# Performance work log

Hardware: AMD Instinct MI355X
Metric: run time of the kernel (lower is better)

The kernel has to match this reference:

```python
import jax, jax.numpy as jnp
import numpy as np

B, N, K, H, D = 2, 8192, 16, 4, 32
C_IN, C_OUT = 64, 128
HD = H * D


def setup_inputs() -> dict:
    key = jax.random.key(0)
    ks = jax.random.split(key, 16)
    s = 0.02
    return {
        "xyzs": jax.random.normal(ks[0], (B, N, 3), jnp.float32),
        "features": jax.random.normal(ks[1], (B, N, C_IN), jnp.float32),
        "k_graph": jax.random.randint(ks[2], (B, N, K), 0, N),
        # projections (stored as [in, out]; torch Linear applies x @ W.T)
        "Wk": jax.random.normal(ks[3], (C_IN, HD), jnp.float32) * s,
        "Wv": jax.random.normal(ks[4], (C_IN, HD), jnp.float32) * s,
        "Wq": jax.random.normal(ks[5], (C_IN, HD), jnp.float32) * s,
        # aggregate MLP: Linear(HD,HD) -> ReLU -> Linear(HD,H)
        "A1": jax.random.normal(ks[6], (HD, HD), jnp.float32) * s,
        "b1": jnp.zeros((HD,), jnp.float32),
        "A2": jax.random.normal(ks[7], (HD, H), jnp.float32) * s,
        "b2": jnp.zeros((H,), jnp.float32),
        # position MLP: Linear(3,3) -> ReLU -> Linear(3,HD)
        "P1": jax.random.normal(ks[8], (3, 3), jnp.float32) * s,
        "bp1": jnp.zeros((3,), jnp.float32),
        "P2": jax.random.normal(ks[9], (3, HD), jnp.float32) * s,
        "bp2": jnp.zeros((HD,), jnp.float32),
        # output projection Linear(HD, C_OUT)
        "Wout": jax.random.normal(ks[10], (HD, C_OUT), jnp.float32) * s,
        "bout": jnp.zeros((C_OUT,), jnp.float32),
    }


def reference(xyzs, features, k_graph, Wk, Wv, Wq, A1, b1, A2, b2,
              P1, bp1, P2, bp2, Wout, bout):
    # KNN gather (irregular access): [B,N,K,*]
    nbr_feat = jax.vmap(lambda f, g: f[g])(features, k_graph)   # [B,N,K,C_IN]
    nbr_xyz = jax.vmap(lambda x, g: x[g])(xyzs, k_graph)        # [B,N,K,3]

    rel_pos = xyzs[:, :, None, :] - nbr_xyz                      # [B,N,K,3]
    pe = jax.nn.relu(rel_pos @ P1 + bp1) @ P2 + bp2              # [B,N,K,HD]

    keys = nbr_feat @ Wk                                         # [B,N,K,HD]
    values = nbr_feat @ Wv                                       # [B,N,K,HD]
    queries = features @ Wq                                      # [B,N,HD]

    # subtraction attention + aggregate MLP -> per-head logits
    attn = queries[:, :, None, :] - keys + pe                    # [B,N,K,HD]
    attn = jax.nn.relu(attn @ A1 + b1) @ A2 + b2                 # [B,N,K,H]
    attn = jax.nn.softmax(attn, axis=-2)                         # softmax over K

    # weighted reduce over neighbors
    fv = (values + pe).reshape(B, N, K, H, D)
    fused = jnp.sum(attn[..., None] * fv, axis=2)                # [B,N,H,D]
    fused = fused.reshape(B, N, HD)
    return fused @ Wout + bout                                   # [B,N,C_OUT]
```

## Files before the change

### kernel.cpp

```cpp
#include <hip/hip_runtime.h>
#include <hip/hip_bf16.h>

#define BATCH 2
#define NPTS  8192
#define BN    (BATCH * NPTS)
#define KNN   16
#define HEADS 4
#define HD    128
#define CIN   64
#define COUT  128
#define WCOLS 384

using short8  = __attribute__((ext_vector_type(8))) short;
using float4v = __attribute__((ext_vector_type(4))) float;

static __device__ __forceinline__ unsigned short f2bf(float x) {
    unsigned u = __float_as_uint(x);
    u += 0x7fffu + ((u >> 16) & 1u);
    return (unsigned short)(u >> 16);
}
static __device__ __forceinline__ float bf_lo(unsigned u) { return __uint_as_float(u << 16); }
static __device__ __forceinline__ float bf_hi(unsigned u) { return __uint_as_float(u & 0xffff0000u); }
static __device__ __forceinline__ unsigned pack2(float a, float b) {
    return (unsigned)f2bf(a) | ((unsigned)f2bf(b) << 16);
}

template <int CTRL>
static __device__ __forceinline__ float dpp_mov(float x) {
    return __int_as_float(
        __builtin_amdgcn_update_dpp(0, __float_as_int(x), CTRL, 0xf, 0xf, false));
}
static __device__ __forceinline__ float ror_sum16(float x) {
    x += dpp_mov<0x128>(x);
    x += dpp_mov<0x124>(x);
    x += dpp_mov<0x122>(x);
    x += dpp_mov<0x121>(x);
    return x;
}
static __device__ __forceinline__ float ror_max16(float x) {
    x = fmaxf(x, dpp_mov<0x128>(x));
    x = fmaxf(x, dpp_mov<0x124>(x));
    x = fmaxf(x, dpp_mov<0x122>(x));
    x = fmaxf(x, dpp_mov<0x121>(x));
    return x;
}

__global__ __launch_bounds__(256) void prep_kernel(
        const float* __restrict__ Wk, const float* __restrict__ Wv,
        const float* __restrict__ Wq, const float* __restrict__ A1,
        const float* __restrict__ b1, const float* __restrict__ P2,
        const float* __restrict__ bp2, const float* __restrict__ Wout,
        unsigned short* __restrict__ WcatT, unsigned short* __restrict__ WoutT,
        float* __restrict__ P2A1, float* __restrict__ cvec) {
    int W = blockIdx.x * 4 + (threadIdx.x >> 6);
    int lane = threadIdx.x & 63;
    if (W < 384) {
        int kk = W / 6, nb = W % 6;
        int n = nb * 64 + lane;
        if (nb < 4) {
            const float* src = (nb < 2 ? Wq : Wk) + kk * HD;
            int jj = n & (HD - 1);
            float acc = 0.f;
            #pragma unroll 8
            for (int m = 0; m < HD; ++m)
                acc += src[m] * A1[m * HD + jj];
            WcatT[n * CIN + kk] = f2bf(acc);
        } else {
            WcatT[n * CIN + kk] = f2bf(Wv[kk * HD + (n - 2 * HD)]);
        }
    } else if (W < 384 + 256) {
        int u = (W - 384) * 64 + lane;
        int n = u >> 7, kk = u & 127;
        WoutT[u] = f2bf(Wout[kk * COUT + n]);
    } else if (W < 646) {
        int u = (W - 640) * 64 + lane;
        int r = u >> 7, j = u & 127;
        const float* src = P2 + r * HD;
        float acc = 0.f;
        #pragma unroll 8
        for (int m = 0; m < HD; ++m)
            acc += src[m] * A1[m * HD + j];
        P2A1[u] = acc;
    } else {
        int j = (W - 646) * 64 + lane;
        float acc = b1[j];
        #pragma unroll 8
        for (int m = 0; m < HD; ++m)
            acc += bp2[m] * A1[m * HD + j];
        cvec[j] = acc;
    }
}

#define AK 88
__global__ __launch_bounds__(256) void qkv_kernel(const float* __restrict__ F,
                                                  const unsigned short* __restrict__ WcatT,
                                                  const float* __restrict__ cvec,
                                                  unsigned short* __restrict__ QKVb) {
    __shared__ unsigned short Af[64 * AK];
    int p0 = blockIdx.x * 64;
    int t = threadIdx.x;

    #pragma unroll
    for (int i = 0; i < 4; ++i) {
        int v = t + i * 256;
        int row = v >> 4, c4 = (v & 15) * 4;
        float4 fa = *(const float4*)(F + (p0 + row) * CIN + c4);
        *(uint2*)(&Af[row * AK + c4]) = make_uint2(pack2(fa.x, fa.y), pack2(fa.z, fa.w));
    }
    __syncthreads();

    int w = t >> 6, l = t & 63;
    int ml = l & 15, quad = l >> 4;
    int n0 = w * 96;

    short8 b[6][2];
    #pragma unroll
    for (int j = 0; j < 6; ++j) {
        int n = n0 + j * 16 + ml;
        b[j][0] = *(const short8*)(WcatT + n * CIN + quad * 8);
        b[j][1] = *(const short8*)(WcatT + n * CIN + 32 + quad * 8);
    }
    short8 a[4][2];
    #pragma unroll
    for (int mt = 0; mt < 4; ++mt) {
        a[mt][0] = *(const short8*)(&Af[(mt * 16 + ml) * AK + quad * 8]);
        a[mt][1] = *(const short8*)(&Af[(mt * 16 + ml) * AK + 32 + quad * 8]);
    }

    #pragma unroll
    for (int j = 0; j < 6; ++j) {
        #pragma unroll
        for (int mt = 0; mt < 4; ++mt) {
            float4v acc = {0.f, 0.f, 0.f, 0.f};
            acc = __builtin_amdgcn_mfma_f32_16x16x32_bf16(b[j][0], a[mt][0], acc, 0, 0, 0);
            acc = __builtin_amdgcn_mfma_f32_16x16x32_bf16(b[j][1], a[mt][1], acc, 0, 0, 0);
            int nc = n0 + j * 16 + quad * 4;
            float c0 = 0.f, c1 = 0.f, c2 = 0.f, c3 = 0.f;
            if (nc < HD) {
                float4 cv = *(const float4*)(cvec + nc);
                c0 = cv.x; c1 = cv.y; c2 = cv.z; c3 = cv.w;
            }
            int row = p0 + mt * 16 + ml;
            *(uint2*)(QKVb + row * WCOLS + nc) =
                make_uint2(pack2(acc[0] + c0, acc[1] + c1),
                           pack2(acc[2] + c2, acc[3] + c3));
        }
    }
}

__global__ __launch_bounds__(256) void attn_kernel(
        const float* __restrict__ xyzs, const int* __restrict__ kg,
        const unsigned short* __restrict__ QKVb,
        const float* __restrict__ P1, const float* __restrict__ bp1,
        const float* __restrict__ P2, const float* __restrict__ bp2,
        const float* __restrict__ P2A1,
        const float* __restrict__ A2, const float* __restrict__ b2,
        unsigned short* __restrict__ FUSEDb) {
    int p = blockIdx.x;
    int b = p >> 13;
    int t = threadIdx.x;
    int g = t >> 4, k = t & 15, c0 = g * 8;
    int w = t >> 6;
    int lane = t & 63;

    __shared__ float4 A2s[HD];
    __shared__ float4 lgp[4][16];
    __shared__ float4 hs16[16];
    __shared__ float  ats[64];
    __shared__ float4 hbf[4];

    if (t < HD) A2s[t] = *(const float4*)(A2 + t * 4);

    int idx = kg[p * KNN + k];
    int q = b * NPTS + idx;

    float r0 = xyzs[p*3+0] - xyzs[q*3+0];
    float r1 = xyzs[p*3+1] - xyzs[q*3+1];
    float r2 = xyzs[p*3+2] - xyzs[q*3+2];
    float h0 = fmaxf(r0*P1[0] + r1*P1[3] + r2*P1[6] + bp1[0], 0.f);
    float h1 = fmaxf(r0*P1[1] + r1*P1[4] + r2*P1[7] + bp1[1], 0.f);
    float h2 = fmaxf(r0*P1[2] + r1*P1[5] + r2*P1[8] + bp1[2], 0.f);
    if (g == 0) hs16[k] = make_float4(h0, h1, h2, 0.f);

    uint4 qu = *(const uint4*)(QKVb + p * WCOLS + c0);
    uint4 ku = *(const uint4*)(QKVb + q * WCOLS + HD + c0);
    uint4 vu = *(const uint4*)(QKVb + q * WCOLS + 2 * HD + c0);

    float qz[8] = { bf_lo(qu.x), bf_hi(qu.x), bf_lo(qu.y), bf_hi(qu.y),
                    bf_lo(qu.z), bf_hi(qu.z), bf_lo(qu.w), bf_hi(qu.w) };
    float kr[8] = { bf_lo(ku.x), bf_hi(ku.x), bf_lo(ku.y), bf_hi(ku.y),
                    bf_lo(ku.z), bf_hi(ku.z), bf_lo(ku.w), bf_hi(ku.w) };

    float wa0[8], wa1[8], wa2[8];
    *(float4*)(wa0)     = *(const float4*)(P2A1 + 0*HD + c0);
    *(float4*)(wa0 + 4) = *(const float4*)(P2A1 + 0*HD + c0 + 4);
    *(float4*)(wa1)     = *(const float4*)(P2A1 + 1*HD + c0);
    *(float4*)(wa1 + 4) = *(const float4*)(P2A1 + 1*HD + c0 + 4);
    *(float4*)(wa2)     = *(const float4*)(P2A1 + 2*HD + c0);
    *(float4*)(wa2 + 4) = *(const float4*)(P2A1 + 2*HD + c0 + 4);

    __syncthreads();

    float pl0 = 0.f, pl1 = 0.f, pl2 = 0.f, pl3 = 0.f;
    #pragma unroll
    for (int j = 0; j < 8; ++j) {
        float z = fmaxf(qz[j] - kr[j] + h0*wa0[j] + h1*wa1[j] + h2*wa2[j], 0.f);
        float4 ar = A2s[c0 + j];
        pl0 += z * ar.x; pl1 += z * ar.y; pl2 += z * ar.z; pl3 += z * ar.w;
    }
    pl0 += __shfl_xor(pl0, 16, 64); pl0 += __shfl_xor(pl0, 32, 64);
    pl1 += __shfl_xor(pl1, 16, 64); pl1 += __shfl_xor(pl1, 32, 64);
    pl2 += __shfl_xor(pl2, 16, 64); pl2 += __shfl_xor(pl2, 32, 64);
    pl3 += __shfl_xor(pl3, 16, 64); pl3 += __shfl_xor(pl3, 32, 64);
    if (lane < 16) lgp[w][lane] = make_float4(pl0, pl1, pl2, pl3);
    __syncthreads();

    if (t < 64) {
        int hh = t >> 4, kk = t & 15;
        const float* lp = (const float*)lgp;
        float lgt = b2[hh] + lp[0*64 + kk*4 + hh] + lp[1*64 + kk*4 + hh]
                           + lp[2*64 + kk*4 + hh] + lp[3*64 + kk*4 + hh];
        float m = ror_max16(lgt);
        float e = __expf(lgt - m);
        float s = ror_sum16(e);
        float a = e / s;
        ats[t] = a;
        float4 hv = hs16[kk];
        float hb0 = ror_sum16(a * hv.x);
        float hb1 = ror_sum16(a * hv.y);
        float hb2 = ror_sum16(a * hv.z);
        if (kk == 0) hbf[hh] = make_float4(hb0, hb1, hb2, 0.f);
    }
    __syncthreads();

    float a = ats[w * 16 + k];
    float vr[8] = { bf_lo(vu.x), bf_hi(vu.x), bf_lo(vu.y), bf_hi(vu.y),
                    bf_lo(vu.z), bf_hi(vu.z), bf_lo(vu.w), bf_hi(vu.w) };
    float wv[8];
    #pragma unroll
    for (int j = 0; j < 8; ++j) wv[j] = ror_sum16(a * vr[j]);

    if (k == 0) {
        float4 hb = hbf[w];
        float q0[8], q1[8], q2[8], bpv[8];
        *(float4*)(q0)     = *(const float4*)(P2 + 0*HD + c0);
        *(float4*)(q0 + 4) = *(const float4*)(P2 + 0*HD + c0 + 4);
        *(float4*)(q1)     = *(const float4*)(P2 + 1*HD + c0);
        *(float4*)(q1 + 4) = *(const float4*)(P2 + 1*HD + c0 + 4);
        *(float4*)(q2)     = *(const float4*)(P2 + 2*HD + c0);
        *(float4*)(q2 + 4) = *(const float4*)(P2 + 2*HD + c0 + 4);
        *(float4*)(bpv)     = *(const float4*)(bp2 + c0);
        *(float4*)(bpv + 4) = *(const float4*)(bp2 + c0 + 4);
        float f[8];
        #pragma unroll
        for (int j = 0; j < 8; ++j)
            f[j] = wv[j] + hb.x*q0[j] + hb.y*q1[j] + hb.z*q2[j] + bpv[j];
        uint4 fu;
        fu.x = pack2(f[0], f[1]); fu.y = pack2(f[2], f[3]);
        fu.z = pack2(f[4], f[5]); fu.w = pack2(f[6], f[7]);
        *(uint4*)(FUSEDb + p * HD + c0) = fu;
    }
}

#define OK2 144
__global__ __launch_bounds__(256) void out_kernel(const unsigned short* __restrict__ FUSEDb,
                                                  const unsigned short* __restrict__ WoutT,
                                                  const float* __restrict__ bout,
                                                  float* __restrict__ out) {
    __shared__ unsigned short Af[64 * OK2];
    int p0 = blockIdx.x * 64;
    int t = threadIdx.x;

    #pragma unroll
    for (int i = 0; i < 4; ++i) {
        int v = t + i * 256;
        int row = v >> 4, c8 = (v & 15) * 8;
        *(uint4*)(&Af[row * OK2 + c8]) = *(const uint4*)(FUSEDb + (p0 + row) * HD + c8);
    }
    __syncthreads();

    int w = t >> 6, l = t & 63;
    int ml = l & 15, quad = l >> 4;
    int n0 = w * 32;

    short8 b[2][4];
    #pragma unroll
    for (int j = 0; j < 2; ++j) {
        int n = n0 + j * 16 + ml;
        #pragma unroll
        for (int ks = 0; ks < 4; ++ks)
            b[j][ks] = *(const short8*)(WoutT + n * HD + ks * 32 + quad * 8);
    }
    short8 a[4][4];
    #pragma unroll
    for (int mt = 0; mt < 4; ++mt)
        #pragma unroll
        for (int ks = 0; ks < 4; ++ks)
            a[mt][ks] = *(const short8*)(&Af[(mt * 16 + ml) * OK2 + ks * 32 + quad * 8]);

    #pragma unroll
    for (int j = 0; j < 2; ++j) {
        int nc = n0 + j * 16 + quad * 4;
        float4 bo = *(const float4*)(bout + nc);
        #pragma unroll
        for (int mt = 0; mt < 4; ++mt) {
            float4v acc = {0.f, 0.f, 0.f, 0.f};
            #pragma unroll
            for (int ks = 0; ks < 4; ++ks)
                acc = __builtin_amdgcn_mfma_f32_16x16x32_bf16(b[j][ks], a[mt][ks], acc, 0, 0, 0);
            int row = p0 + mt * 16 + ml;
            *(float4*)(out + row * COUT + nc) =
                make_float4(acc[0] + bo.x, acc[1] + bo.y, acc[2] + bo.z, acc[3] + bo.w);
        }
    }
}

extern "C" void kernel_launch(void* const* d_in, const int* in_sizes, int n_in,
                              void* d_out, int out_size, void* d_ws, size_t ws_size,
                              hipStream_t stream) {
    const float* xyzs = (const float*)d_in[0];
    const float* feat = (const float*)d_in[1];
    const int*   kg   = (const int*)  d_in[2];
    const float* Wk   = (const float*)d_in[3];
    const float* Wv   = (const float*)d_in[4];
    const float* Wq   = (const float*)d_in[5];
    const float* A1   = (const float*)d_in[6];
    const float* b1   = (const float*)d_in[7];
    const float* A2   = (const float*)d_in[8];
    const float* b2   = (const float*)d_in[9];
    const float* P1   = (const float*)d_in[10];
    const float* bp1  = (const float*)d_in[11];
    const float* P2   = (const float*)d_in[12];
    const float* bp2  = (const float*)d_in[13];
    const float* Wout = (const float*)d_in[14];
    const float* bout = (const float*)d_in[15];
    float* out = (float*)d_out;

    float* ws = (float*)d_ws;
    float* cvec = ws;
    float* P2A1 = ws + 128;
    unsigned short* QKVb  = (unsigned short*)(ws + 512);
    unsigned short* FUSEDb = QKVb + (size_t)BN * WCOLS;
    unsigned short* WcatT = FUSEDb + (size_t)BN * HD;
    unsigned short* WoutT = WcatT + WCOLS * CIN;

    prep_kernel<<<162, 256, 0, stream>>>(
        Wk, Wv, Wq, A1, b1, P2, bp2, Wout, WcatT, WoutT, P2A1, cvec);

    qkv_kernel<<<BN / 64, 256, 0, stream>>>(feat, WcatT, cvec, QKVb);

    attn_kernel<<<BN, 256, 0, stream>>>(
        xyzs, kg, QKVb, P1, bp1, P2, bp2, P2A1, A2, b2, FUSEDb);

    out_kernel<<<BN / 64, 256, 0, stream>>>(FUSEDb, WoutT, bout, out);
}
```

Baseline: 161.8 us.

## Fuse all four stages into one cooperative persistent kernel with grid syncs

Adds a cooperative mega-kernel of 1024 blocks that runs weight prep, QKV projection, attention and the output projection in sequence, with grid.sync between phases. Each block owns 16 points, prefetches the next point's neighbour data in software, and keeps fused results in LDS for an in-block MFMA output projection. This removes the launch gaps and the FUSED round-trip through global memory. In exchange it processes points serially per block with two block barriers per point, uses fewer blocks than the old one-block-per-point attention grid, and only runs if the occupancy check passes; otherwise it falls back to the four-kernel path.

```diff
diff --git a/kernel.cpp b/kernel.cpp
--- a/kernel.cpp
+++ b/kernel.cpp
@@ -1,5 +1,8 @@
 #include <hip/hip_runtime.h>
 #include <hip/hip_bf16.h>
+#include <hip/hip_cooperative_groups.h>
+
+namespace cg = cooperative_groups;
 
 #define BATCH 2
 #define NPTS  8192
@@ -43,6 +46,246 @@
     x = fmaxf(x, dpp_mov<0x122>(x));
     x = fmaxf(x, dpp_mov<0x121>(x));
     return x;
+}
+
+__global__ __launch_bounds__(256, 4) void mega_kernel(
+        const float* __restrict__ xyzs, const float* __restrict__ feat,
+        const int* __restrict__ kg,
+        const float* __restrict__ Wk, const float* __restrict__ Wv,
+        const float* __restrict__ Wq, const float* __restrict__ A1,
+        const float* __restrict__ b1, const float* __restrict__ A2,
+        const float* __restrict__ b2, const float* __restrict__ P1,
+        const float* __restrict__ bp1, const float* __restrict__ P2,
+        const float* __restrict__ bp2, const float* __restrict__ Wout,
+        const float* __restrict__ bout,
+        unsigned short* __restrict__ WcatT, unsigned short* __restrict__ WoutT,
+        float* __restrict__ P2A1, float* __restrict__ cvec,
+        unsigned short* __restrict__ QKVb, float* __restrict__ out) {
+    cg::grid_group grid = cg::this_grid();
+    int t = threadIdx.x;
+    int bid = blockIdx.x;
+    int w = t >> 6, lane = t & 63;
+
+    __shared__ unsigned short Af[16 * 88];
+    __shared__ float4 A2s[HD];
+    __shared__ float4 lgp[2][4][16];
+    __shared__ float4 hs16[2][16];
+    __shared__ float  ats[2][64];
+    __shared__ float4 hbf[2][4];
+    __shared__ unsigned short fusedLDS[16 * 136];
+
+    {
+        int W = bid * 4 + w;
+        if (W < 384) {
+            int kk = W / 6, nb = W % 6;
+            int n = nb * 64 + lane;
+            if (nb < 4) {
+                const float* src = (nb < 2 ? Wq : Wk) + kk * HD;
+                int jj = n & (HD - 1);
+                float acc = 0.f;
+                #pragma unroll 8
+                for (int m = 0; m < HD; ++m) acc += src[m] * A1[m * HD + jj];
+                WcatT[n * CIN + kk] = f2bf(acc);
+            } else {
+                WcatT[n * CIN + kk] = f2bf(Wv[kk * HD + (n - 2 * HD)]);
+            }
+        } else if (W < 640) {
+            int u = (W - 384) * 64 + lane;
+            int n = u >> 7, kk = u & 127;
+            WoutT[u] = f2bf(Wout[kk * COUT + n]);
+        } else if (W < 646) {
+            int u = (W - 640) * 64 + lane;
+            int r = u >> 7, jj = u & 127;
+            const float* src = P2 + r * HD;
+            float acc = 0.f;
+            #pragma unroll 8
+            for (int m = 0; m < HD; ++m) acc += src[m] * A1[m * HD + jj];
+            P2A1[u] = acc;
+        } else if (W < 648) {
+            int jj = (W - 646) * 64 + lane;
+            float acc = b1[jj];
+            #pragma unroll 8
+            for (int m = 0; m < HD; ++m) acc += bp2[m] * A1[m * HD + jj];
+            cvec[jj] = acc;
+        }
+    }
+    grid.sync();
+
+    int p0 = bid * 16;
+    {
+        {
+            int row = t >> 4, c4 = (t & 15) * 4;
+            float4 fa = *(const float4*)(feat + (p0 + row) * CIN + c4);
+            *(uint2*)(&Af[row * 88 + c4]) =
+                make_uint2(pack2(fa.x, fa.y), pack2(fa.z, fa.w));
+        }
+        __syncthreads();
+        int ml = lane & 15, quad = lane >> 4;
+        int n0 = w * 96;
+        short8 a0 = *(const short8*)(&Af[ml * 88 + quad * 8]);
+        short8 a1 = *(const short8*)(&Af[ml * 88 + 32 + quad * 8]);
+        #pragma unroll
+        for (int j = 0; j < 6; ++j) {
+            int n = n0 + j * 16 + ml;
+            short8 bf0 = *(const short8*)(WcatT + n * CIN + quad * 8);
+            short8 bf1 = *(const short8*)(WcatT + n * CIN + 32 + quad * 8);
+            float4v acc = {0.f, 0.f, 0.f, 0.f};
+            acc = __builtin_amdgcn_mfma_f32_16x16x32_bf16(bf0, a0, acc, 0, 0, 0);
+            acc = __builtin_amdgcn_mfma_f32_16x16x32_bf16(bf1, a1, acc, 0, 0, 0);
+            int nc = n0 + j * 16 + quad * 4;
+            float c0 = 0.f, c1 = 0.f, c2 = 0.f, c3 = 0.f;
+            if (nc < HD) {
+                float4 cv = *(const float4*)(cvec + nc);
+                c0 = cv.x; c1 = cv.y; c2 = cv.z; c3 = cv.w;
+            }
+            *(uint2*)(QKVb + (p0 + ml) * WCOLS + nc) =
+                make_uint2(pack2(acc[0] + c0, acc[1] + c1),
+                           pack2(acc[2] + c2, acc[3] + c3));
+        }
+    }
+    grid.sync();
+
+    {
+        int b = p0 >> 13;
+        int g = t >> 4, k = t & 15, c0g = g * 8;
+
+        if (t < HD) A2s[t] = *(const float4*)(A2 + t * 4);
+
+        float wa0[8], wa1[8], wa2[8];
+        *(float4*)(wa0)     = *(const float4*)(P2A1 + 0*HD + c0g);
+        *(float4*)(wa0 + 4) = *(const float4*)(P2A1 + 0*HD + c0g + 4);
+        *(float4*)(wa1)     = *(const float4*)(P2A1 + 1*HD + c0g);
+        *(float4*)(wa1 + 4) = *(const float4*)(P2A1 + 1*HD + c0g + 4);
+        *(float4*)(wa2)     = *(const float4*)(P2A1 + 2*HD + c0g);
+        *(float4*)(wa2 + 4) = *(const float4*)(P2A1 + 2*HD + c0g + 4);
+        __syncthreads();
+
+        int p = p0;
+        int idx = kg[p * KNN + k];
+        int q = b * NPTS + idx;
+        float xp0 = xyzs[p*3+0], xp1 = xyzs[p*3+1], xp2 = xyzs[p*3+2];
+        float xn0 = xyzs[q*3+0], xn1 = xyzs[q*3+1], xn2 = xyzs[q*3+2];
+        uint4 qu = *(const uint4*)(QKVb + p * WCOLS + c0g);
+        uint4 ku = *(const uint4*)(QKVb + q * WCOLS + HD + c0g);
+        uint4 vu = *(const uint4*)(QKVb + q * WCOLS + 2 * HD + c0g);
+
+        for (int j = 0; j < 16; ++j) {
+            int pr = j & 1;
+            float r0 = xp0 - xn0, r1 = xp1 - xn1, r2 = xp2 - xn2;
+            float h0 = fmaxf(r0*P1[0] + r1*P1[3] + r2*P1[6] + bp1[0], 0.f);
+            float h1 = fmaxf(r0*P1[1] + r1*P1[4] + r2*P1[7] + bp1[1], 0.f);
+            float h2 = fmaxf(r0*P1[2] + r1*P1[5] + r2*P1[8] + bp1[2], 0.f);
+            if (g == 0) hs16[pr][k] = make_float4(h0, h1, h2, 0.f);
+
+            int idxN = 0;
+            if (j < 15) idxN = kg[(p + 1) * KNN + k];
+
+            float qz[8] = { bf_lo(qu.x), bf_hi(qu.x), bf_lo(qu.y), bf_hi(qu.y),
+                            bf_lo(qu.z), bf_hi(qu.z), bf_lo(qu.w), bf_hi(qu.w) };
+            float kr[8] = { bf_lo(ku.x), bf_hi(ku.x), bf_lo(ku.y), bf_hi(ku.y),
+                            bf_lo(ku.z), bf_hi(ku.z), bf_lo(ku.w), bf_hi(ku.w) };
+            float pl0 = 0.f, pl1 = 0.f, pl2 = 0.f, pl3 = 0.f;
+            #pragma unroll
+            for (int jj = 0; jj < 8; ++jj) {
+                float z = fmaxf(qz[jj] - kr[jj] + h0*wa0[jj] + h1*wa1[jj] + h2*wa2[jj], 0.f);
+                float4 ar = A2s[c0g + jj];
+                pl0 += z * ar.x; pl1 += z * ar.y; pl2 += z * ar.z; pl3 += z * ar.w;
+            }
+            pl0 += __shfl_xor(pl0, 16, 64); pl0 += __shfl_xor(pl0, 32, 64);
+            pl1 += __shfl_xor(pl1, 16, 64); pl1 += __shfl_xor(pl1, 32, 64);
+            pl2 += __shfl_xor(pl2, 16, 64); pl2 += __shfl_xor(pl2, 32, 64);
+            pl3 += __shfl_xor(pl3, 16, 64); pl3 += __shfl_xor(pl3, 32, 64);
+            if (lane < 16) lgp[pr][w][lane] = make_float4(pl0, pl1, pl2, pl3);
+            __syncthreads();
+
+            if (t < 64) {
+                int hh = t >> 4, kk = t & 15;
+                const float* lp = (const float*)&lgp[pr][0][0];
+                float lgt = b2[hh] + lp[0*64 + kk*4 + hh] + lp[1*64 + kk*4 + hh]
+                                   + lp[2*64 + kk*4 + hh] + lp[3*64 + kk*4 + hh];
+                float m = ror_max16(lgt);
+                float e = __expf(lgt - m);
+                float s = ror_sum16(e);
+                float a = e / s;
+                ats[pr][t] = a;
+                float4 hv = hs16[pr][kk];
+                float hb0 = ror_sum16(a * hv.x);
+                float hb1 = ror_sum16(a * hv.y);
+                float hb2 = ror_sum16(a * hv.z);
+                if (kk == 0) hbf[pr][hh] = make_float4(hb0, hb1, hb2, 0.f);
+            }
+
+            uint4 quN, kuN, vuN;
+            float xp0N = 0.f, xp1N = 0.f, xp2N = 0.f;
+            float xn0N = 0.f, xn1N = 0.f, xn2N = 0.f;
+            int qN = b * NPTS + idxN;
+            if (j < 15) {
+                int pn = p + 1;
+                xp0N = xyzs[pn*3+0]; xp1N = xyzs[pn*3+1]; xp2N = xyzs[pn*3+2];
+                xn0N = xyzs[qN*3+0]; xn1N = xyzs[qN*3+1]; xn2N = xyzs[qN*3+2];
+                quN = *(const uint4*)(QKVb + pn * WCOLS + c0g);
+                kuN = *(const uint4*)(QKVb + qN * WCOLS + HD + c0g);
+                vuN = *(const uint4*)(QKVb + qN * WCOLS + 2 * HD + c0g);
+            }
+            __syncthreads();
+
+            float a = ats[pr][w * 16 + k];
+            float vr[8] = { bf_lo(vu.x), bf_hi(vu.x), bf_lo(vu.y), bf_hi(vu.y),
+                            bf_lo(vu.z), bf_hi(vu.z), bf_lo(vu.w), bf_hi(vu.w) };
+            float wv[8];
+            #pragma unroll
+            for (int jj = 0; jj < 8; ++jj) wv[jj] = ror_sum16(a * vr[jj]);
+
+            if (k == 0) {
+                float4 hb = hbf[pr][w];
+                float q0[8], q1[8], q2[8], bpv[8];
+                *(float4*)(q0)     = *(const float4*)(P2 + 0*HD + c0g);
+                *(float4*)(q0 + 4) = *(const float4*)(P2 + 0*HD + c0g + 4);
+                *(float4*)(q1)     = *(const float4*)(P2 + 1*HD + c0g);
+                *(float4*)(q1 + 4) = *(const float4*)(P2 + 1*HD + c0g + 4);
+                *(float4*)(q2)     = *(const float4*)(P2 + 2*HD + c0g);
+                *(float4*)(q2 + 4) = *(const float4*)(P2 + 2*HD + c0g + 4);
+                *(float4*)(bpv)     = *(const float4*)(bp2 + c0g);
+                *(float4*)(bpv + 4) = *(const float4*)(bp2 + c0g + 4);
+                float f[8];
+                #pragma unroll
+                for (int jj = 0; jj < 8; ++jj)
+                    f[jj] = wv[jj] + hb.x*q0[jj] + hb.y*q1[jj] + hb.z*q2[jj] + bpv[jj];
+                uint4 fu;
+                fu.x = pack2(f[0], f[1]); fu.y = pack2(f[2], f[3]);
+                fu.z = pack2(f[4], f[5]); fu.w = pack2(f[6], f[7]);
+                *(uint4*)(&fusedLDS[j * 136 + c0g]) = fu;
+            }
+
+            p += 1; q = qN;
+            qu = quN; ku = kuN; vu = vuN;
+            xp0 = xp0N; xp1 = xp1N; xp2 = xp2N;
+            xn0 = xn0N; xn1 = xn1N; xn2 = xn2N;
+        }
+        __syncthreads();
+
+        int ml = lane & 15, quad = lane >> 4;
+        short8 afr[4];
+        #pragma unroll
+        for (int ks = 0; ks < 4; ++ks)
+            afr[ks] = *(const short8*)(&fusedLDS[ml * 136 + ks * 32 + quad * 8]);
+        int n0 = w * 32;
+        #pragma unroll
+        for (int jn = 0; jn < 2; ++jn) {
+            int n = n0 + jn * 16 + ml;
+            float4v acc = {0.f, 0.f, 0.f, 0.f};
+            #pragma unroll
+            for (int ks = 0; ks < 4; ++ks) {
+                short8 bfr = *(const short8*)(WoutT + n * HD + ks * 32 + quad * 8);
+                acc = __builtin_amdgcn_mfma_f32_16x16x32_bf16(bfr, afr[ks], acc, 0, 0, 0);
+            }
+            int nc = n0 + jn * 16 + quad * 4;
+            float4 bo = *(const float4*)(bout + nc);
+            *(float4*)(out + (p0 + ml) * COUT + nc) =
+                make_float4(acc[0] + bo.x, acc[1] + bo.y,
+                            acc[2] + bo.z, acc[3] + bo.w);
+        }
+    }
 }
 
 __global__ __launch_bounds__(256) void prep_kernel(
@@ -62,13 +305,12 @@
             int jj = n & (HD - 1);
             float acc = 0.f;
             #pragma unroll 8
-            for (int m = 0; m < HD; ++m)
-                acc += src[m] * A1[m * HD + jj];
+            for (int m = 0; m < HD; ++m) acc += src[m] * A1[m * HD + jj];
             WcatT[n * CIN + kk] = f2bf(acc);
         } else {
             WcatT[n * CIN + kk] = f2bf(Wv[kk * HD + (n - 2 * HD)]);
         }
-    } else if (W < 384 + 256) {
+    } else if (W < 640) {
         int u = (W - 384) * 64 + lane;
         int n = u >> 7, kk = u & 127;
         WoutT[u] = f2bf(Wout[kk * COUT + n]);
@@ -78,15 +320,13 @@
         const float* src = P2 + r * HD;
         float acc = 0.f;
         #pragma unroll 8
-        for (int m = 0; m < HD; ++m)
-            acc += src[m] * A1[m * HD + j];
+        for (int m = 0; m < HD; ++m) acc += src[m] * A1[m * HD + j];
         P2A1[u] = acc;
-    } else {
+    } else if (W < 648) {
         int j = (W - 646) * 64 + lane;
         float acc = b1[j];
         #pragma unroll 8
-        for (int m = 0; m < HD; ++m)
-            acc += bp2[m] * A1[m * HD + j];
+        for (int m = 0; m < HD; ++m) acc += bp2[m] * A1[m * HD + j];
         cvec[j] = acc;
     }
 }
@@ -99,7 +339,6 @@
     __shared__ unsigned short Af[64 * AK];
     int p0 = blockIdx.x * 64;
     int t = threadIdx.x;
-
     #pragma unroll
     for (int i = 0; i < 4; ++i) {
         int v = t + i * 256;
@@ -108,11 +347,9 @@
         *(uint2*)(&Af[row * AK + c4]) = make_uint2(pack2(fa.x, fa.y), pack2(fa.z, fa.w));
     }
     __syncthreads();
-
     int w = t >> 6, l = t & 63;
     int ml = l & 15, quad = l >> 4;
     int n0 = w * 96;
-
     short8 b[6][2];
     #pragma unroll
     for (int j = 0; j < 6; ++j) {
@@ -126,7 +363,6 @@
         a[mt][0] = *(const short8*)(&Af[(mt * 16 + ml) * AK + quad * 8]);
         a[mt][1] = *(const short8*)(&Af[(mt * 16 + ml) * AK + 32 + quad * 8]);
     }
-
     #pragma unroll
     for (int j = 0; j < 6; ++j) {
         #pragma unroll
@@ -270,7 +506,6 @@
     __shared__ unsigned short Af[64 * OK2];
     int p0 = blockIdx.x * 64;
     int t = threadIdx.x;
-
     #pragma unroll
     for (int i = 0; i < 4; ++i) {
         int v = t + i * 256;
@@ -278,11 +513,9 @@
         *(uint4*)(&Af[row * OK2 + c8]) = *(const uint4*)(FUSEDb + (p0 + row) * HD + c8);
     }
     __syncthreads();
-
     int w = t >> 6, l = t & 63;
     int ml = l & 15, quad = l >> 4;
     int n0 = w * 32;
-
     short8 b[2][4];
     #pragma unroll
     for (int j = 0; j < 2; ++j) {
@@ -297,7 +530,6 @@
         #pragma unroll
         for (int ks = 0; ks < 4; ++ks)
             a[mt][ks] = *(const short8*)(&Af[(mt * 16 + ml) * OK2 + ks * 32 + quad * 8]);
-
     #pragma unroll
     for (int j = 0; j < 2; ++j) {
         int nc = n0 + j * 16 + quad * 4;
@@ -339,18 +571,37 @@
     float* ws = (float*)d_ws;
     float* cvec = ws;
     float* P2A1 = ws + 128;
-    unsigned short* QKVb  = (unsigned short*)(ws + 512);
-    unsigned short* FUSEDb = QKVb + (size_t)BN * WCOLS;
-    unsigned short* WcatT = FUSEDb + (size_t)BN * HD;
-    unsigned short* WoutT = WcatT + WCOLS * CIN;
-
-    prep_kernel<<<162, 256, 0, stream>>>(
-        Wk, Wv, Wq, A1, b1, P2, bp2, Wout, WcatT, WoutT, P2A1, cvec);
-
-    qkv_kernel<<<BN / 64, 256, 0, stream>>>(feat, WcatT, cvec, QKVb);
-
-    attn_kernel<<<BN, 256, 0, stream>>>(
-        xyzs, kg, QKVb, P1, bp1, P2, bp2, P2A1, A2, b2, FUSEDb);
-
-    out_kernel<<<BN / 64, 256, 0, stream>>>(FUSEDb, WoutT, bout, out);
-}
+    unsigned short* QKVb   = (unsigned short*)(ws + 512);
+    unsigned short* WcatT  = QKVb + (size_t)BN * WCOLS;
+    unsigned short* WoutT  = WcatT + WCOLS * CIN;
+    unsigned short* FUSEDb = WoutT + COUT * HD;
+
+    int nb = 0;
+    bool use_coop =
+        (hipOccupancyMaxActiveBlocksPerMultiprocessor(&nb, mega_kernel, 256, 0)
+             == hipSuccess) && nb >= 4;
+
+    if (use_coop) {
+        void* args[] = {
+            (void*)&xyzs, (void*)&feat, (void*)&kg,
+            (void*)&Wk, (void*)&Wv, (void*)&Wq, (void*)&A1, (void*)&b1,
+            (void*)&A2, (void*)&b2, (void*)&P1, (void*)&bp1, (void*)&P2,
+            (void*)&bp2, (void*)&Wout, (void*)&bout,
+            (void*)&WcatT, (void*)&WoutT, (void*)&P2A1, (void*)&cvec,
+            (void*)&QKVb, (void*)&out
+        };
+        if (hipLaunchCooperativeKernel((const void*)mega_kernel,
+                                       dim3(1024), dim3(256), args, 0, stream)
+                != hipSuccess)
+            use_coop = false;
+    }
+
+    if (!use_coop) {
+        prep_kernel<<<162, 256, 0, stream>>>(
+            Wk, Wv, Wq, A1, b1, P2, bp2, Wout, WcatT, WoutT, P2A1, cvec);
+        qkv_kernel<<<BN / 64, 256, 0, stream>>>(feat, WcatT, cvec, QKVb);
+        attn_kernel<<<BN, 256, 0, stream>>>(
+            xyzs, kg, QKVb, P1, bp1, P2, bp2, P2A1, A2, b2, FUSEDb);
+        out_kernel<<<BN / 64, 256, 0, stream>>>(FUSEDb, WoutT, bout, out);
+    }
+}
```

New measurement: 161.8 us. No clear change (-0.0%).
